# Kernel tuning notes

Measured on AMD Instinct MI355X. Metric: run time of the kernel, lower is better.

Reference implementation:

```python
import jax, jax.numpy as jnp
import numpy as np

EPS = 1e-5


def clin(xr, xi, Wr, Wi, br, bi):
    # complex linear layer: (xr + i xi) @ (Wr + i Wi) + (br + i bi)
    yr = xr @ Wr - xi @ Wi + br
    yi = xr @ Wi + xi @ Wr + bi
    return yr, yi


def setup_inputs() -> dict:
    key = jax.random.key(0)
    ks = jax.random.split(key, 16)
    B, N, DE, DV = 4, 256, 128, 64
    s_in = 1.0 / np.sqrt(DE)
    s_p = 1.0 / np.sqrt(DV)
    f32 = jnp.float32
    inp = {
        'Z_q': jax.random.normal(ks[0], (B, 2, N, DE), f32),
        'Z_k': jax.random.normal(ks[1], (B, 2, N, DE), f32),
        'Z_v': jax.random.normal(ks[2], (B, 2, N, DE), f32),
        't_measure_all': jnp.tile(jnp.arange(N + 1, dtype=f32) * 0.01, (B, 1)),
        'Wq_r': jax.random.normal(ks[3], (DE, DV), f32) * s_in,
        'Wq_i': jax.random.normal(ks[4], (DE, DV), f32) * s_in,
        'bq_r': jnp.zeros((DV,), f32), 'bq_i': jnp.zeros((DV,), f32),
        'Wk_r': jax.random.normal(ks[5], (DE, DV), f32) * s_in,
        'Wk_i': jax.random.normal(ks[6], (DE, DV), f32) * s_in,
        'bk_r': jnp.zeros((DV,), f32), 'bk_i': jnp.zeros((DV,), f32),
        'Wv_r': jax.random.normal(ks[7], (DE, DV), f32) * s_in,
        'Wv_i': jax.random.normal(ks[8], (DE, DV), f32) * s_in,
        'bv_r': jnp.zeros((DV,), f32), 'bv_i': jnp.zeros((DV,), f32),
        'Wp_r': jax.random.normal(ks[9], (DV, DE), f32) * s_p,
        'Wp_i': jax.random.normal(ks[10], (DV, DE), f32) * s_p,
        'bp_r': jnp.zeros((DE,), f32), 'bp_i': jnp.zeros((DE,), f32),
        'lambda1': jax.random.normal(ks[11], (2, DV // 2), f32),
        'lambda_Omega_sqrt': jax.random.normal(ks[12], (DV,), f32) / DV,
        'lambda_Gamma_sqrt': jax.random.normal(ks[13], (DV,), f32) / DV,
        'noise_floor': jnp.array(1.0, f32),
        'tau': jnp.array(1.0, f32),
        'nu': jnp.array(1.0, f32),
        'eta_param': jnp.zeros((DV,), f32),
    }
    return inp


def reference(Z_q, Z_k, Z_v, t_measure_all,
              Wq_r, Wq_i, bq_r, bq_i, Wk_r, Wk_i, bk_r, bk_i,
              Wv_r, Wv_i, bv_r, bv_i, Wp_r, Wp_i, bp_r, bp_i,
              lambda1, lambda_Omega_sqrt, lambda_Gamma_sqrt,
              noise_floor, tau, nu, eta_param):
    N = Z_q.shape[2]
    # complex projections (B, N, d)
    Qr, Qi = clin(Z_q[:, 0], Z_q[:, 1], Wq_r, Wq_i, bq_r, bq_i)
    Kr_, Ki_ = clin(Z_k[:, 0], Z_k[:, 1], Wk_r, Wk_i, bk_r, bk_i)
    Vr, Vi = clin(Z_v[:, 0], Z_v[:, 1], Wv_r, Wv_i, bv_r, bv_i)
    # state-transition eigenvalues: stable conjugate pairs
    re = jnp.concatenate([-lambda1[0] ** 2, -lambda1[0] ** 2])  # (d_v,), Re<=0
    im = jnp.concatenate([lambda1[1], -lambda1[1]])             # (d_v,)
    lam_Om = lambda_Omega_sqrt ** 2
    lam_Ga = lambda_Gamma_sqrt ** 2 + EPS
    # pairwise complex exponential kernel exp(lambda * (t_i - t_j))
    t = t_measure_all[0, :-1]                       # (N,)
    dt = t[:, None] - t[None, :]                    # (N, N)
    amp = jnp.exp(re[None, None, :] * dt[:, :, None])
    ph = im[None, None, :] * dt[:, :, None]
    Ker = amp * jnp.cos(ph)                          # (N, N, d_v)
    Kei = amp * jnp.sin(ph)
    # propagated value estimates Z_hat_ij = exp(lam dt_ij) * V_j
    Zhr = Ker[None] * Vr[:, None] - Kei[None] * Vi[:, None]  # (B, N, N, d_v)
    Zhi = Ker[None] * Vi[:, None] + Kei[None] * Vr[:, None]
    # residuals R_ij = Q_i - exp(lam dt_ij) * K_j
    Rr = Qr[:, :, None, :] - (Ker[None] * Kr_[:, None] - Kei[None] * Ki_[:, None])
    Ri = Qi[:, :, None, :] - (Ker[None] * Ki_[:, None] + Kei[None] * Kr_[:, None])
    # per-pair covariance (OU-process propagation of measurement + process noise)
    adt = jnp.abs(dt)[:, :, None]
    exp2 = jnp.exp(2.0 * re * adt)                   # (N, N, d_v)
    Vij = lam_Ga * exp2 + lam_Om * (exp2 - 1.0) / (2.0 * (re - EPS))
    # mahalanobis distance and attention scores
    mah = (Rr ** 2 + Ri ** 2) / (Vij[None] + lam_Ga)          # (B, N, N, d_v)
    dist_sum = jnp.abs(nu) * jnp.sum(mah, axis=3, keepdims=True)
    base = Vij[None] * (noise_floor + dist_sum + EPS)
    scores = -jnp.abs(tau) * jnp.log(base)
    mask = jnp.tril(jnp.ones((N, N), bool))
    scores = jnp.where(mask[None, :, :, None], scores, -jnp.inf)
    Qij = jax.nn.softmax(scores, axis=2)             # normalize over j
    m = mask[None, :, :, None].astype(Zhr.dtype)
    Zhr = Zhr * m
    Zhi = Zhi * m
    est_vr = jnp.einsum('bijd,bijd->bid', Qij, Zhr)
    est_vi = jnp.einsum('bijd,bijd->bid', Qij, Zhi)
    # gated residual mix (double sigmoid as in source)
    eta = jax.nn.sigmoid(eta_param)
    g = jax.nn.sigmoid(eta)
    elr = (1.0 - eta) * Vr + g * est_vr
    eli = (1.0 - eta) * Vi + g * est_vi
    # one-step-ahead prediction via matrix exponential exp(lambda * h)
    h = t[1] - t[0]
    ma = jnp.exp(re * h)
    mr, mi = ma * jnp.cos(im * h), ma * jnp.sin(im * h)
    ppr = mr * elr - mi * eli
    ppi = mr * eli + mi * elr
    outr, outi = clin(ppr, ppi, Wp_r, Wp_i, bp_r, bp_i)
    est_latent = jnp.stack([elr, eli], axis=1)       # (B, 2, N, d_v)
    out = jnp.stack([outr, outi], axis=1)            # (B, 2, N, d_e)
    Zhat = jnp.stack([Zhr, Zhi], axis=1)             # (B, 2, N, N, d_v)
    lambda_h = jnp.stack([re, im])                   # (2, d_v)
    return est_latent, out, Qij, Zhat, lambda_h
```

## Files before the change

### kernel.cpp

```cpp
#include <hip/hip_runtime.h>
#include <math.h>

#define B_ 4
#define N_ 256
#define DE_ 128
#define DV_ 64
#define EPS_ 1e-5f

typedef __attribute__((ext_vector_type(4))) float f32x4;

__device__ __forceinline__ f32x4 ld4(const float* p) { return *(const f32x4*)p; }
__device__ __forceinline__ void st4(float* p, f32x4 v) { *(f32x4*)p = v; }
__device__ __forceinline__ void nt4(float* p, f32x4 v) { __builtin_nontemporal_store(v, (f32x4*)p); }
__device__ __forceinline__ f32x4 exp4(f32x4 a) {
    f32x4 r; r[0]=expf(a[0]); r[1]=expf(a[1]); r[2]=expf(a[2]); r[3]=expf(a[3]); return r;
}
__device__ __forceinline__ f32x4 max4(f32x4 a, f32x4 b) {
    f32x4 r; r[0]=fmaxf(a[0],b[0]); r[1]=fmaxf(a[1],b[1]); r[2]=fmaxf(a[2],b[2]); r[3]=fmaxf(a[3],b[3]); return r;
}
__device__ __forceinline__ f32x4 log4(f32x4 a) {
    f32x4 r; r[0]=logf(a[0]); r[1]=logf(a[1]); r[2]=logf(a[2]); r[3]=logf(a[3]); return r;
}

#define OFF_ETA   0
#define OFF_G     64
#define OFF_MR    128
#define OFF_MI    192
#define OFF_KER   256
#define OFF_KEI   (OFF_KER + N_*DV_)
#define OFF_LOGV  (OFF_KEI + N_*DV_)
#define OFF_INV   (OFF_LOGV + N_*DV_)
#define OFF_QR    (OFF_INV + N_*DV_)
#define OFF_QI    (OFF_QR + B_*N_*DV_)
#define OFF_KR    (OFF_QI + B_*N_*DV_)
#define OFF_KI    (OFF_KR + B_*N_*DV_)
#define OFF_VR    (OFF_KI + B_*N_*DV_)
#define OFF_VI    (OFF_VR + B_*N_*DV_)

#define OUT_EL    0
#define OUT_OUT   (B_*2*N_*DV_)
#define OUT_QIJ   (OUT_OUT + B_*2*N_*DE_)
#define OUT_ZHAT  (OUT_QIJ + B_*N_*N_*DV_)
#define OUT_LAMH  (OUT_ZHAT + (size_t)B_*2*N_*N_*DV_)

__global__ __launch_bounds__(256) void k_pre(
    const float* __restrict__ Zq, const float* __restrict__ Zk, const float* __restrict__ Zv,
    const float* __restrict__ Wqr, const float* __restrict__ Wqi,
    const float* __restrict__ bqr, const float* __restrict__ bqi,
    const float* __restrict__ Wkr, const float* __restrict__ Wki,
    const float* __restrict__ bkr, const float* __restrict__ bki,
    const float* __restrict__ Wvr, const float* __restrict__ Wvi,
    const float* __restrict__ bvr, const float* __restrict__ bvi,
    const float* __restrict__ t,  const float* __restrict__ lam1,
    const float* __restrict__ lOm, const float* __restrict__ lGa,
    const float* __restrict__ eta_p,
    float* __restrict__ ws, float* __restrict__ out)
{
    const int tid = (int)threadIdx.x;
    const int w = tid >> 6;
    const int d = tid & 63;

    if (blockIdx.x >= 256) {
        const int idx = (int)blockIdx.x - 256;
        const int delta = idx * 4 + w;

        const float l0 = lam1[d & 31];
        const float re = -l0 * l0;
        const float im = (d < 32) ? lam1[32 + d] : -lam1[d];

        const float lo = lOm[d];
        const float lam_Om = lo * lo;
        const float lg_ = lGa[d];
        const float lam_Ga = lg_ * lg_ + EPS_;

        const float t0 = t[0];
        const float dt = t[delta] - t0;

        const float amp = expf(re * dt);
        const float ph  = im * dt;
        const int td = delta * DV_ + d;
        ws[OFF_KER + td] = amp * cosf(ph);
        ws[OFF_KEI + td] = amp * sinf(ph);

        const float e2  = expf(2.0f * re * dt);
        const float vij = lam_Ga * e2 + lam_Om * (e2 - 1.0f) / (2.0f * (re - EPS_));
        ws[OFF_LOGV + td] = logf(vij);
        ws[OFF_INV  + td] = 1.0f / (vij + lam_Ga);

        if (delta == 0) {
            const float eta = 1.0f / (1.0f + expf(-eta_p[d]));
            const float g   = 1.0f / (1.0f + expf(-eta));
            ws[OFF_ETA + d] = eta;
            ws[OFF_G   + d] = g;
            const float h  = t[1] - t0;
            const float ma = expf(re * h);
            ws[OFF_MR + d] = ma * cosf(im * h);
            ws[OFF_MI + d] = ma * sinf(im * h);
            out[OUT_LAMH + d]       = re;
            out[OUT_LAMH + DV_ + d] = im;
        }
        return;
    }

    const int row0 = (int)blockIdx.x * 4;
    const int b = row0 >> 8;
    const int n0 = row0 & (N_ - 1);

    __shared__ float x[4][6][DE_];
    #pragma unroll
    for (int it = 0; it < 3; ++it) {
        const int v = tid + it * 256;
        const int seg = v >> 5;
        const int pos = v & 31;
        const int r = seg & 3;
        const int a = seg >> 2;
        const int m = a >> 1;
        const int c = a & 1;
        const float* src = (m == 0) ? Zq : ((m == 1) ? Zk : Zv);
        const f32x4 val = ld4(src + ((size_t)(b*2 + c)*N_ + (n0 + r))*DE_ + pos*4);
        st4(&x[r][a][pos*4], val);
    }
    __syncthreads();

    const int row = row0 + w;
    float aqr = 0.f, aqi = 0.f, akr = 0.f, aki = 0.f, avr = 0.f, avi = 0.f;
    #pragma unroll 8
    for (int k = 0; k < DE_; ++k) {
        const float xqr = x[w][0][k], xqi = x[w][1][k];
        const float xkr = x[w][2][k], xki = x[w][3][k];
        const float xvr = x[w][4][k], xvi = x[w][5][k];
        float wr, wi;
        wr = Wqr[k*DV_ + d]; wi = Wqi[k*DV_ + d];
        aqr += xqr*wr - xqi*wi; aqi += xqr*wi + xqi*wr;
        wr = Wkr[k*DV_ + d]; wi = Wki[k*DV_ + d];
        akr += xkr*wr - xki*wi; aki += xkr*wi + xki*wr;
        wr = Wvr[k*DV_ + d]; wi = Wvi[k*DV_ + d];
        avr += xvr*wr - xvi*wi; avi += xvr*wi + xvi*wr;
    }
    const int o = row * DV_ + d;
    ws[OFF_QR + o] = aqr + bqr[d];
    ws[OFF_QI + o] = aqi + bqi[d];
    ws[OFF_KR + o] = akr + bkr[d];
    ws[OFF_KI + o] = aki + bki[d];
    ws[OFF_VR + o] = avr + bvr[d];
    ws[OFF_VI + o] = avi + bvi[d];
}

__global__ __launch_bounds__(256) void k_main2(
    const float* __restrict__ ws, float* __restrict__ out,
    const float* __restrict__ Wpr, const float* __restrict__ Wpi,
    const float* __restrict__ bpr, const float* __restrict__ bpi,
    const float* __restrict__ nf_p, const float* __restrict__ tau_p,
    const float* __restrict__ nu_p)
{
    const int vb = (int)blockIdx.x;
    const int b = vb & 3;
    const int i = (N_ - 1) - (vb >> 2);
    const int row = b * N_ + i;
    const int tid = (int)threadIdx.x;
    const int w = tid >> 6;
    const int l = tid & 63;
    const int g = l >> 4;
    const int q16 = l & 15;
    const int dq = q16 * 4;

    __shared__ float lb[N_];
    __shared__ f32x4 redM[4][16];
    __shared__ f32x4 redS[4][16];
    __shared__ f32x4 redR[4][16];
    __shared__ f32x4 redI[4][16];
    __shared__ float ppr_s[DV_], ppi_s[DV_];

    const float nf    = nf_p[0];
    const float tau_a = fabsf(tau_p[0]);
    const float nu_a  = fabsf(nu_p[0]);

    const f32x4 qr4 = ld4(ws + OFF_QR + row*DV_ + dq);
    const f32x4 qi4 = ld4(ws + OFF_QI + row*DV_ + dq);

    const int nfull = (i + 1) >> 2;
    const int tail  = (i + 1) & 3;
    const f32x4 z4 = {0.f,0.f,0.f,0.f};

    float* qij = out + OUT_QIJ + (size_t)row * N_ * DV_;
    float* zro = out + OUT_ZHAT + ((size_t)(b*2+0)*N_ + i) * N_ * DV_;
    float* zio = out + OUT_ZHAT + ((size_t)(b*2+1)*N_ + i) * N_ * DV_;

    f32x4 m4 = {-3.0e38f, -3.0e38f, -3.0e38f, -3.0e38f};
    f32x4 s4 = {0.f, 0.f, 0.f, 0.f};
    #pragma unroll 2
    for (int T = w; T < nfull; T += 4) {
        const int j = 4*T + g;
        const int o = j*DV_ + dq;
        const int td = (i - j)*DV_ + dq;
        const f32x4 ker = ld4(ws + OFF_KER  + td);
        const f32x4 kei = ld4(ws + OFF_KEI  + td);
        const f32x4 vnv = ld4(ws + OFF_INV  + td);
        const f32x4 lgv = ld4(ws + OFF_LOGV + td);
        const int kj = (b*N_ + j)*DV_ + dq;
        const f32x4 kr = ld4(ws + OFF_KR + kj);
        const f32x4 ki = ld4(ws + OFF_KI + kj);
        const f32x4 vr = ld4(ws + OFF_VR + kj);
        const f32x4 vi = ld4(ws + OFF_VI + kj);
        const f32x4 rr = qr4 - (ker*kr - kei*ki);
        const f32x4 ri = qi4 - (ker*ki + kei*kr);
        const f32x4 mah = (rr*rr + ri*ri) * vnv;
        float ds = mah[0] + mah[1] + mah[2] + mah[3];
        ds += __shfl_xor(ds, 1);
        ds += __shfl_xor(ds, 2);
        ds += __shfl_xor(ds, 4);
        ds += __shfl_xor(ds, 8);
        const float lg = logf(nf + nu_a*ds + EPS_);
        if (q16 == 0) lb[j] = lg;
        const f32x4 sc = (-tau_a) * (lgv + lg);
        const f32x4 mn = max4(m4, sc);
        s4 = s4 * exp4(m4 - mn) + exp4(sc - mn);
        m4 = mn;
        const f32x4 zr = ker*vr - kei*vi;
        const f32x4 zi = ker*vi + kei*vr;
        nt4(zro + o, zr);
        nt4(zio + o, zi);
    }
    if (tail && ((nfull & 3) == w)) {
        const int j = 4*nfull + g;
        const int o = j*DV_ + dq;
        const bool act = (g < tail);
        const int td = (act ? (i - j) : 0)*DV_ + dq;
        const f32x4 ker = ld4(ws + OFF_KER  + td);
        const f32x4 kei = ld4(ws + OFF_KEI  + td);
        const f32x4 vnv = ld4(ws + OFF_INV  + td);
        const f32x4 lgv = ld4(ws + OFF_LOGV + td);
        const int kj = (b*N_ + (act ? j : 0))*DV_ + dq;
        const f32x4 kr = ld4(ws + OFF_KR + kj);
        const f32x4 ki = ld4(ws + OFF_KI + kj);
        const f32x4 vr = ld4(ws + OFF_VR + kj);
        const f32x4 vi = ld4(ws + OFF_VI + kj);
        const f32x4 rr = qr4 - (ker*kr - kei*ki);
        const f32x4 ri = qi4 - (ker*ki + kei*kr);
        const f32x4 mah = (rr*rr + ri*ri) * vnv;
        float ds = mah[0] + mah[1] + mah[2] + mah[3];
        ds += __shfl_xor(ds, 1);
        ds += __shfl_xor(ds, 2);
        ds += __shfl_xor(ds, 4);
        ds += __shfl_xor(ds, 8);
        const float lg = logf(nf + nu_a*ds + EPS_);
        if (act) {
            if (q16 == 0) lb[j] = lg;
            const f32x4 sc = (-tau_a) * (lgv + lg);
            const f32x4 mn = max4(m4, sc);
            s4 = s4 * exp4(m4 - mn) + exp4(sc - mn);
            m4 = mn;
            const f32x4 zr = ker*vr - kei*vi;
            const f32x4 zi = ker*vi + kei*vr;
            nt4(zro + o, zr);
            nt4(zio + o, zi);
        } else {
            nt4(zro + o, z4);
            nt4(zio + o, z4);
        }
    }
    {
        const int jz0 = 4 * (nfull + (tail ? 1 : 0));
        const int nq = (N_ - jz0) * 16;
        for (int u = tid; u < nq; u += 256) {
            const int o = jz0*DV_ + u*4;
            nt4(zro + o, z4);
            nt4(zio + o, z4);
        }
    }

    #pragma unroll
    for (int mask = 16; mask <= 32; mask <<= 1) {
        f32x4 mo, so;
        #pragma unroll
        for (int c = 0; c < 4; ++c) { mo[c] = __shfl_xor(m4[c], mask); so[c] = __shfl_xor(s4[c], mask); }
        const f32x4 mn = max4(m4, mo);
        s4 = s4 * exp4(m4 - mn) + so * exp4(mo - mn);
        m4 = mn;
    }
    if (g == 0) { redM[w][q16] = m4; redS[w][q16] = s4; }
    __syncthreads();
    f32x4 M = redM[0][q16], S = redS[0][q16];
    #pragma unroll
    for (int w2 = 1; w2 < 4; ++w2) {
        const f32x4 mo = redM[w2][q16], so = redS[w2][q16];
        const f32x4 mn = max4(M, mo);
        S = S * exp4(M - mn) + so * exp4(mo - mn);
        M = mn;
    }
    const f32x4 C = M + log4(S);

    f32x4 evr = {0.f,0.f,0.f,0.f}, evi = {0.f,0.f,0.f,0.f};
    #pragma unroll 2
    for (int T = w; T < nfull; T += 4) {
        const int j = 4*T + g;
        const int o = j*DV_ + dq;
        const int td = (i - j)*DV_ + dq;
        const f32x4 lgv = ld4(ws + OFF_LOGV + td);
        const f32x4 ker = ld4(ws + OFF_KER + td);
        const f32x4 kei = ld4(ws + OFF_KEI + td);
        const float lg = lb[j];
        const f32x4 q4 = exp4((-tau_a)*(lgv + lg) - C);
        nt4(qij + o, q4);
        const int vj = (b*N_ + j)*DV_ + dq;
        const f32x4 vr = ld4(ws + OFF_VR + vj);
        const f32x4 vi = ld4(ws + OFF_VI + vj);
        evr += q4 * (ker*vr - kei*vi);
        evi += q4 * (ker*vi + kei*vr);
    }
    if (tail && ((nfull & 3) == w)) {
        const int j = 4*nfull + g;
        const int o = j*DV_ + dq;
        if (g < tail) {
            const int td = (i - j)*DV_ + dq;
            const f32x4 lgv = ld4(ws + OFF_LOGV + td);
            const f32x4 ker = ld4(ws + OFF_KER + td);
            const f32x4 kei = ld4(ws + OFF_KEI + td);
            const float lg = lb[j];
            const f32x4 q4 = exp4((-tau_a)*(lgv + lg) - C);
            nt4(qij + o, q4);
            const int vj = (b*N_ + j)*DV_ + dq;
            const f32x4 vr = ld4(ws + OFF_VR + vj);
            const f32x4 vi = ld4(ws + OFF_VI + vj);
            evr += q4 * (ker*vr - kei*vi);
            evi += q4 * (ker*vi + kei*vr);
        } else {
            nt4(qij + o, z4);
        }
    }
    {
        const int jz0 = 4 * (nfull + (tail ? 1 : 0));
        const int nq = (N_ - jz0) * 16;
        for (int u = tid; u < nq; u += 256) {
            nt4(qij + jz0*DV_ + u*4, z4);
        }
    }

    #pragma unroll
    for (int mask = 16; mask <= 32; mask <<= 1) {
        #pragma unroll
        for (int c = 0; c < 4; ++c) {
            evr[c] += __shfl_xor(evr[c], mask);
            evi[c] += __shfl_xor(evi[c], mask);
        }
    }
    if (g == 0) { redR[w][q16] = evr; redI[w][q16] = evi; }
    __syncthreads();

    if (tid < 16) {
        const f32x4 Evr = redR[0][tid] + redR[1][tid] + redR[2][tid] + redR[3][tid];
        const f32x4 Evi = redI[0][tid] + redI[1][tid] + redI[2][tid] + redI[3][tid];
        const int dq2 = tid * 4;
        const f32x4 vr  = ld4(ws + OFF_VR + row*DV_ + dq2);
        const f32x4 vi  = ld4(ws + OFF_VI + row*DV_ + dq2);
        const f32x4 eta = ld4(ws + OFF_ETA + dq2);
        const f32x4 gg  = ld4(ws + OFF_G + dq2);
        const f32x4 elr = (1.0f - eta)*vr + gg*Evr;
        const f32x4 eli = (1.0f - eta)*vi + gg*Evi;
        st4(out + OUT_EL + ((size_t)(b*2+0)*N_ + i)*DV_ + dq2, elr);
        st4(out + OUT_EL + ((size_t)(b*2+1)*N_ + i)*DV_ + dq2, eli);
        const f32x4 mr = ld4(ws + OFF_MR + dq2);
        const f32x4 mi = ld4(ws + OFF_MI + dq2);
        st4(ppr_s + dq2, mr*elr - mi*eli);
        st4(ppi_s + dq2, mr*eli + mi*elr);
    }
    __syncthreads();

    if (tid < DE_) {
        const int e = tid;
        float ar = bpr[e], ai = bpi[e];
        #pragma unroll 8
        for (int dd = 0; dd < DV_; ++dd) {
            const float wr = Wpr[dd*DE_ + e], wi = Wpi[dd*DE_ + e];
            const float r = ppr_s[dd], im = ppi_s[dd];
            ar += r*wr - im*wi;
            ai += r*wi + im*wr;
        }
        out[OUT_OUT + ((size_t)(b*2+0)*N_ + i)*DE_ + e] = ar;
        out[OUT_OUT + ((size_t)(b*2+1)*N_ + i)*DE_ + e] = ai;
    }
}

extern "C" void kernel_launch(void* const* d_in, const int* in_sizes, int n_in,
                              void* d_out, int out_size, void* d_ws, size_t ws_size,
                              hipStream_t stream)
{
    const float* Zq   = (const float*)d_in[0];
    const float* Zk   = (const float*)d_in[1];
    const float* Zv   = (const float*)d_in[2];
    const float* t    = (const float*)d_in[3];
    const float* Wqr  = (const float*)d_in[4];
    const float* Wqi  = (const float*)d_in[5];
    const float* bqr  = (const float*)d_in[6];
    const float* bqi  = (const float*)d_in[7];
    const float* Wkr  = (const float*)d_in[8];
    const float* Wki  = (const float*)d_in[9];
    const float* bkr  = (const float*)d_in[10];
    const float* bki  = (const float*)d_in[11];
    const float* Wvr  = (const float*)d_in[12];
    const float* Wvi  = (const float*)d_in[13];
    const float* bvr  = (const float*)d_in[14];
    const float* bvi  = (const float*)d_in[15];
    const float* Wpr  = (const float*)d_in[16];
    const float* Wpi  = (const float*)d_in[17];
    const float* bpr  = (const float*)d_in[18];
    const float* bpi  = (const float*)d_in[19];
    const float* lam1 = (const float*)d_in[20];
    const float* lOm  = (const float*)d_in[21];
    const float* lGa  = (const float*)d_in[22];
    const float* nf   = (const float*)d_in[23];
    const float* tau  = (const float*)d_in[24];
    const float* nu   = (const float*)d_in[25];
    const float* etap = (const float*)d_in[26];

    float* ws  = (float*)d_ws;
    float* out = (float*)d_out;

    k_pre<<<256 + 64, 256, 0, stream>>>(Zq, Zk, Zv,
                                        Wqr, Wqi, bqr, bqi,
                                        Wkr, Wki, bkr, bki,
                                        Wvr, Wvi, bvr, bvi,
                                        t, lam1, lOm, lGa, etap, ws, out);
    k_main2<<<B_*N_, 256, 0, stream>>>(ws, out, Wpr, Wpi, bpr, bpi, nf, tau, nu);
}
```

Measured before the change: 72.98 us.

## Factor softmax weights into precomputed products and fuse value accumulation into first pass

Drops the online max-subtracted softmax. The score exponent is split into a per-delta factor A = vij^-tau, precomputed in the prep kernel, and a per-j factor w_j = (nf+nu*ds)^-tau. The first pass then accumulates unnormalized sums for the normalizer and the weighted Zhat, so the second pass only writes the normalized Qij and no longer reloads kernel and V values or calls exp. Without max subtraction it risks overflow or underflow when the scores have a large dynamic range.

```diff
diff --git a/kernel.cpp b/kernel.cpp
--- a/kernel.cpp
+++ b/kernel.cpp
@@ -12,15 +12,6 @@
 __device__ __forceinline__ f32x4 ld4(const float* p) { return *(const f32x4*)p; }
 __device__ __forceinline__ void st4(float* p, f32x4 v) { *(f32x4*)p = v; }
 __device__ __forceinline__ void nt4(float* p, f32x4 v) { __builtin_nontemporal_store(v, (f32x4*)p); }
-__device__ __forceinline__ f32x4 exp4(f32x4 a) {
-    f32x4 r; r[0]=expf(a[0]); r[1]=expf(a[1]); r[2]=expf(a[2]); r[3]=expf(a[3]); return r;
-}
-__device__ __forceinline__ f32x4 max4(f32x4 a, f32x4 b) {
-    f32x4 r; r[0]=fmaxf(a[0],b[0]); r[1]=fmaxf(a[1],b[1]); r[2]=fmaxf(a[2],b[2]); r[3]=fmaxf(a[3],b[3]); return r;
-}
-__device__ __forceinline__ f32x4 log4(f32x4 a) {
-    f32x4 r; r[0]=logf(a[0]); r[1]=logf(a[1]); r[2]=logf(a[2]); r[3]=logf(a[3]); return r;
-}
 
 #define OFF_ETA   0
 #define OFF_G     64
@@ -28,8 +19,8 @@
 #define OFF_MI    192
 #define OFF_KER   256
 #define OFF_KEI   (OFF_KER + N_*DV_)
-#define OFF_LOGV  (OFF_KEI + N_*DV_)
-#define OFF_INV   (OFF_LOGV + N_*DV_)
+#define OFF_A     (OFF_KEI + N_*DV_)
+#define OFF_INV   (OFF_A + N_*DV_)
 #define OFF_QR    (OFF_INV + N_*DV_)
 #define OFF_QI    (OFF_QR + B_*N_*DV_)
 #define OFF_KR    (OFF_QI + B_*N_*DV_)
@@ -53,16 +44,16 @@
     const float* __restrict__ bvr, const float* __restrict__ bvi,
     const float* __restrict__ t,  const float* __restrict__ lam1,
     const float* __restrict__ lOm, const float* __restrict__ lGa,
-    const float* __restrict__ eta_p,
+    const float* __restrict__ eta_p, const float* __restrict__ tau_p,
     float* __restrict__ ws, float* __restrict__ out)
 {
     const int tid = (int)threadIdx.x;
-    const int w = tid >> 6;
+    const int wv = tid >> 6;
     const int d = tid & 63;
 
     if (blockIdx.x >= 256) {
         const int idx = (int)blockIdx.x - 256;
-        const int delta = idx * 4 + w;
+        const int delta = idx * 4 + wv;
 
         const float l0 = lam1[d & 31];
         const float re = -l0 * l0;
@@ -72,6 +63,7 @@
         const float lam_Om = lo * lo;
         const float lg_ = lGa[d];
         const float lam_Ga = lg_ * lg_ + EPS_;
+        const float tau_a = fabsf(tau_p[0]);
 
         const float t0 = t[0];
         const float dt = t[delta] - t0;
@@ -84,8 +76,8 @@
 
         const float e2  = expf(2.0f * re * dt);
         const float vij = lam_Ga * e2 + lam_Om * (e2 - 1.0f) / (2.0f * (re - EPS_));
-        ws[OFF_LOGV + td] = logf(vij);
-        ws[OFF_INV  + td] = 1.0f / (vij + lam_Ga);
+        ws[OFF_A   + td] = expf(-tau_a * logf(vij));
+        ws[OFF_INV + td] = 1.0f / (vij + lam_Ga);
 
         if (delta == 0) {
             const float eta = 1.0f / (1.0f + expf(-eta_p[d]));
@@ -122,13 +114,13 @@
     }
     __syncthreads();
 
-    const int row = row0 + w;
+    const int row = row0 + wv;
     float aqr = 0.f, aqi = 0.f, akr = 0.f, aki = 0.f, avr = 0.f, avi = 0.f;
     #pragma unroll 8
     for (int k = 0; k < DE_; ++k) {
-        const float xqr = x[w][0][k], xqi = x[w][1][k];
-        const float xkr = x[w][2][k], xki = x[w][3][k];
-        const float xvr = x[w][4][k], xvi = x[w][5][k];
+        const float xqr = x[wv][0][k], xqi = x[wv][1][k];
+        const float xkr = x[wv][2][k], xki = x[wv][3][k];
+        const float xvr = x[wv][4][k], xvi = x[wv][5][k];
         float wr, wi;
         wr = Wqr[k*DV_ + d]; wi = Wqi[k*DV_ + d];
         aqr += xqr*wr - xqi*wi; aqi += xqr*wi + xqi*wr;
@@ -158,14 +150,13 @@
     const int i = (N_ - 1) - (vb >> 2);
     const int row = b * N_ + i;
     const int tid = (int)threadIdx.x;
-    const int w = tid >> 6;
+    const int wv = tid >> 6;
     const int l = tid & 63;
     const int g = l >> 4;
     const int q16 = l & 15;
     const int dq = q16 * 4;
 
-    __shared__ float lb[N_];
-    __shared__ f32x4 redM[4][16];
+    __shared__ float wl[N_];
     __shared__ f32x4 redS[4][16];
     __shared__ f32x4 redR[4][16];
     __shared__ f32x4 redI[4][16];
@@ -186,17 +177,18 @@
     float* zro = out + OUT_ZHAT + ((size_t)(b*2+0)*N_ + i) * N_ * DV_;
     float* zio = out + OUT_ZHAT + ((size_t)(b*2+1)*N_ + i) * N_ * DV_;
 
-    f32x4 m4 = {-3.0e38f, -3.0e38f, -3.0e38f, -3.0e38f};
-    f32x4 s4 = {0.f, 0.f, 0.f, 0.f};
+    f32x4 s4  = {0.f,0.f,0.f,0.f};
+    f32x4 evr = {0.f,0.f,0.f,0.f};
+    f32x4 evi = {0.f,0.f,0.f,0.f};
     #pragma unroll 2
-    for (int T = w; T < nfull; T += 4) {
+    for (int T = wv; T < nfull; T += 4) {
         const int j = 4*T + g;
         const int o = j*DV_ + dq;
         const int td = (i - j)*DV_ + dq;
-        const f32x4 ker = ld4(ws + OFF_KER  + td);
-        const f32x4 kei = ld4(ws + OFF_KEI  + td);
-        const f32x4 vnv = ld4(ws + OFF_INV  + td);
-        const f32x4 lgv = ld4(ws + OFF_LOGV + td);
+        const f32x4 ker = ld4(ws + OFF_KER + td);
+        const f32x4 kei = ld4(ws + OFF_KEI + td);
+        const f32x4 vnv = ld4(ws + OFF_INV + td);
+        const f32x4 a4  = ld4(ws + OFF_A   + td);
         const int kj = (b*N_ + j)*DV_ + dq;
         const f32x4 kr = ld4(ws + OFF_KR + kj);
         const f32x4 ki = ld4(ws + OFF_KI + kj);
@@ -210,26 +202,26 @@
         ds += __shfl_xor(ds, 2);
         ds += __shfl_xor(ds, 4);
         ds += __shfl_xor(ds, 8);
-        const float lg = logf(nf + nu_a*ds + EPS_);
-        if (q16 == 0) lb[j] = lg;
-        const f32x4 sc = (-tau_a) * (lgv + lg);
-        const f32x4 mn = max4(m4, sc);
-        s4 = s4 * exp4(m4 - mn) + exp4(sc - mn);
-        m4 = mn;
+        const float wj = expf(-tau_a * logf(nf + nu_a*ds + EPS_));
+        if (q16 == 0) wl[j] = wj;
         const f32x4 zr = ker*vr - kei*vi;
         const f32x4 zi = ker*vi + kei*vr;
         nt4(zro + o, zr);
         nt4(zio + o, zi);
-    }
-    if (tail && ((nfull & 3) == w)) {
+        const f32x4 qn = a4 * wj;
+        s4  += qn;
+        evr += qn * zr;
+        evi += qn * zi;
+    }
+    if (tail && ((nfull & 3) == wv)) {
         const int j = 4*nfull + g;
         const int o = j*DV_ + dq;
         const bool act = (g < tail);
         const int td = (act ? (i - j) : 0)*DV_ + dq;
-        const f32x4 ker = ld4(ws + OFF_KER  + td);
-        const f32x4 kei = ld4(ws + OFF_KEI  + td);
-        const f32x4 vnv = ld4(ws + OFF_INV  + td);
-        const f32x4 lgv = ld4(ws + OFF_LOGV + td);
+        const f32x4 ker = ld4(ws + OFF_KER + td);
+        const f32x4 kei = ld4(ws + OFF_KEI + td);
+        const f32x4 vnv = ld4(ws + OFF_INV + td);
+        const f32x4 a4  = ld4(ws + OFF_A   + td);
         const int kj = (b*N_ + (act ? j : 0))*DV_ + dq;
         const f32x4 kr = ld4(ws + OFF_KR + kj);
         const f32x4 ki = ld4(ws + OFF_KI + kj);
@@ -243,17 +235,17 @@
         ds += __shfl_xor(ds, 2);
         ds += __shfl_xor(ds, 4);
         ds += __shfl_xor(ds, 8);
-        const float lg = logf(nf + nu_a*ds + EPS_);
         if (act) {
-            if (q16 == 0) lb[j] = lg;
-            const f32x4 sc = (-tau_a) * (lgv + lg);
-            const f32x4 mn = max4(m4, sc);
-            s4 = s4 * exp4(m4 - mn) + exp4(sc - mn);
-            m4 = mn;
+            const float wj = expf(-tau_a * logf(nf + nu_a*ds + EPS_));
+            if (q16 == 0) wl[j] = wj;
             const f32x4 zr = ker*vr - kei*vi;
             const f32x4 zi = ker*vi + kei*vr;
             nt4(zro + o, zr);
             nt4(zio + o, zi);
+            const f32x4 qn = a4 * wj;
+            s4  += qn;
+            evr += qn * zr;
+            evi += qn * zi;
         } else {
             nt4(zro + o, z4);
             nt4(zio + o, z4);
@@ -271,59 +263,34 @@
 
     #pragma unroll
     for (int mask = 16; mask <= 32; mask <<= 1) {
-        f32x4 mo, so;
         #pragma unroll
-        for (int c = 0; c < 4; ++c) { mo[c] = __shfl_xor(m4[c], mask); so[c] = __shfl_xor(s4[c], mask); }
-        const f32x4 mn = max4(m4, mo);
-        s4 = s4 * exp4(m4 - mn) + so * exp4(mo - mn);
-        m4 = mn;
-    }
-    if (g == 0) { redM[w][q16] = m4; redS[w][q16] = s4; }
+        for (int c = 0; c < 4; ++c) {
+            s4[c]  += __shfl_xor(s4[c],  mask);
+            evr[c] += __shfl_xor(evr[c], mask);
+            evi[c] += __shfl_xor(evi[c], mask);
+        }
+    }
+    if (g == 0) { redS[wv][q16] = s4; redR[wv][q16] = evr; redI[wv][q16] = evi; }
     __syncthreads();
-    f32x4 M = redM[0][q16], S = redS[0][q16];
-    #pragma unroll
-    for (int w2 = 1; w2 < 4; ++w2) {
-        const f32x4 mo = redM[w2][q16], so = redS[w2][q16];
-        const f32x4 mn = max4(M, mo);
-        S = S * exp4(M - mn) + so * exp4(mo - mn);
-        M = mn;
-    }
-    const f32x4 C = M + log4(S);
-
-    f32x4 evr = {0.f,0.f,0.f,0.f}, evi = {0.f,0.f,0.f,0.f};
+    const f32x4 Z = redS[0][q16] + redS[1][q16] + redS[2][q16] + redS[3][q16];
+    const f32x4 one = {1.f,1.f,1.f,1.f};
+    const f32x4 invZ = one / Z;
+
     #pragma unroll 2
-    for (int T = w; T < nfull; T += 4) {
+    for (int T = wv; T < nfull; T += 4) {
         const int j = 4*T + g;
         const int o = j*DV_ + dq;
         const int td = (i - j)*DV_ + dq;
-        const f32x4 lgv = ld4(ws + OFF_LOGV + td);
-        const f32x4 ker = ld4(ws + OFF_KER + td);
-        const f32x4 kei = ld4(ws + OFF_KEI + td);
-        const float lg = lb[j];
-        const f32x4 q4 = exp4((-tau_a)*(lgv + lg) - C);
+        const f32x4 q4 = ld4(ws + OFF_A + td) * wl[j] * invZ;
         nt4(qij + o, q4);
-        const int vj = (b*N_ + j)*DV_ + dq;
-        const f32x4 vr = ld4(ws + OFF_VR + vj);
-        const f32x4 vi = ld4(ws + OFF_VI + vj);
-        evr += q4 * (ker*vr - kei*vi);
-        evi += q4 * (ker*vi + kei*vr);
-    }
-    if (tail && ((nfull & 3) == w)) {
+    }
+    if (tail && ((nfull & 3) == wv)) {
         const int j = 4*nfull + g;
         const int o = j*DV_ + dq;
         if (g < tail) {
             const int td = (i - j)*DV_ + dq;
-            const f32x4 lgv = ld4(ws + OFF_LOGV + td);
-            const f32x4 ker = ld4(ws + OFF_KER + td);
-            const f32x4 kei = ld4(ws + OFF_KEI + td);
-            const float lg = lb[j];
-            const f32x4 q4 = exp4((-tau_a)*(lgv + lg) - C);
+            const f32x4 q4 = ld4(ws + OFF_A + td) * wl[j] * invZ;
             nt4(qij + o, q4);
-            const int vj = (b*N_ + j)*DV_ + dq;
-            const f32x4 vr = ld4(ws + OFF_VR + vj);
-            const f32x4 vi = ld4(ws + OFF_VI + vj);
-            evr += q4 * (ker*vr - kei*vi);
-            evi += q4 * (ker*vi + kei*vr);
         } else {
             nt4(qij + o, z4);
         }
@@ -336,20 +303,11 @@
         }
     }
 
-    #pragma unroll
-    for (int mask = 16; mask <= 32; mask <<= 1) {
-        #pragma unroll
-        for (int c = 0; c < 4; ++c) {
-            evr[c] += __shfl_xor(evr[c], mask);
-            evi[c] += __shfl_xor(evi[c], mask);
-        }
-    }
-    if (g == 0) { redR[w][q16] = evr; redI[w][q16] = evi; }
-    __syncthreads();
-
     if (tid < 16) {
-        const f32x4 Evr = redR[0][tid] + redR[1][tid] + redR[2][tid] + redR[3][tid];
-        const f32x4 Evi = redI[0][tid] + redI[1][tid] + redI[2][tid] + redI[3][tid];
+        const f32x4 Zt = redS[0][tid] + redS[1][tid] + redS[2][tid] + redS[3][tid];
+        const f32x4 iZ = one / Zt;
+        const f32x4 Evr = (redR[0][tid] + redR[1][tid] + redR[2][tid] + redR[3][tid]) * iZ;
+        const f32x4 Evi = (redI[0][tid] + redI[1][tid] + redI[2][tid] + redI[3][tid]) * iZ;
         const int dq2 = tid * 4;
         const f32x4 vr  = ld4(ws + OFF_VR + row*DV_ + dq2);
         const f32x4 vi  = ld4(ws + OFF_VI + row*DV_ + dq2);
@@ -420,6 +378,6 @@
                                         Wqr, Wqi, bqr, bqi,
                                         Wkr, Wki, bkr, bki,
                                         Wvr, Wvi, bvr, bvi,
-                                        t, lam1, lOm, lGa, etap, ws, out);
+                                        t, lam1, lOm, lGa, etap, tau, ws, out);
     k_main2<<<B_*N_, 256, 0, stream>>>(ws, out, Wpr, Wpi, bpr, bpi, nf, tau, nu);
 }
```

After: 68.25 us. 1.07x faster.
